# Kernel tuning notes

Measured on AMD Instinct MI355X. Metric: run time of the kernel, lower is better.

## Reference

```python
import jax, jax.numpy as jnp
import numpy as np

D_MODEL = 2048
N_HEADS = 16
HEAD_DIM = D_MODEL // N_HEADS
D_FF = 4 * D_MODEL
BATCH = 2
SEQ = 2048
LN_EPS = 1e-5


def setup_inputs() -> dict:
    key = jax.random.key(0)
    ks = jax.random.split(key, 12)
    s = 0.02
    return {
        "x": jax.random.normal(ks[0], (BATCH, SEQ, D_MODEL), dtype=jnp.float32),
        "alibi_bias": jax.random.normal(ks[1], (N_HEADS, SEQ, SEQ), dtype=jnp.float32),
        "W_q": jax.random.normal(ks[2], (D_MODEL, D_MODEL), dtype=jnp.float32) * s,
        "W_k": jax.random.normal(ks[3], (D_MODEL, D_MODEL), dtype=jnp.float32) * s,
        "W_v": jax.random.normal(ks[4], (D_MODEL, D_MODEL), dtype=jnp.float32) * s,
        "W_o": jax.random.normal(ks[5], (D_MODEL, D_MODEL), dtype=jnp.float32) * s,
        "ln1_g": jnp.ones((D_MODEL,), dtype=jnp.float32),
        "ln1_b": jnp.zeros((D_MODEL,), dtype=jnp.float32),
        "ln2_g": jnp.ones((D_MODEL,), dtype=jnp.float32),
        "ln2_b": jnp.zeros((D_MODEL,), dtype=jnp.float32),
        "ffn_w1": jax.random.normal(ks[6], (D_MODEL, D_FF), dtype=jnp.float32) * s,
        "ffn_b1": jnp.zeros((D_FF,), dtype=jnp.float32),
        "ffn_w2": jax.random.normal(ks[7], (D_FF, D_MODEL), dtype=jnp.float32) * s,
        "ffn_b2": jnp.zeros((D_MODEL,), dtype=jnp.float32),
    }


def _layernorm(x, g, b):
    mu = jnp.mean(x, axis=-1, keepdims=True)
    var = jnp.mean(jnp.square(x - mu), axis=-1, keepdims=True)
    return (x - mu) * jax.lax.rsqrt(var + LN_EPS) * g + b


def _mha(x, alibi_bias, W_q, W_k, W_v, W_o):
    B, S, _ = x.shape
    # nn.Linear applies x @ W.T; here W_* are stored as (in, out) so plain matmul.
    q = (x @ W_q).reshape(B, S, N_HEADS, HEAD_DIM).transpose(0, 2, 1, 3)
    k = (x @ W_k).reshape(B, S, N_HEADS, HEAD_DIM).transpose(0, 2, 1, 3)
    v = (x @ W_v).reshape(B, S, N_HEADS, HEAD_DIM).transpose(0, 2, 1, 3)
    q = q / np.sqrt(HEAD_DIM).astype(np.float32)
    scores = jnp.einsum("bhqd,bhkd->bhqk", q, k)  # [B,H,S,S]
    scores = scores + alibi_bias[None]
    causal = jnp.triu(jnp.ones((S, S), dtype=bool), k=1)
    scores = jnp.where(causal, jnp.finfo(scores.dtype).min, scores)
    attn = jax.nn.softmax(scores, axis=-1)
    out = jnp.einsum("bhqk,bhkd->bhqd", attn, v)
    out = out.transpose(0, 2, 1, 3).reshape(B, S, D_MODEL)
    return out @ W_o


def reference(x, alibi_bias, W_q, W_k, W_v, W_o, ln1_g, ln1_b, ln2_g, ln2_b,
              ffn_w1, ffn_b1, ffn_w2, ffn_b2):
    # Attention block (pre-LN, residual); dropout is identity in eval mode.
    h = x + _mha(_layernorm(x, ln1_g, ln1_b), alibi_bias, W_q, W_k, W_v, W_o)
    # FFN block
    n2 = _layernorm(h, ln2_g, ln2_b)
    ffn = jax.nn.gelu(n2 @ ffn_w1 + ffn_b1, approximate=False) @ ffn_w2 + ffn_b2
    return h + ffn
```

## Files before the change

kernel.cpp:

```cpp
#include <hip/hip_runtime.h>
#include <math.h>

#define DM   2048
#define DFF  8192
#define NH   16
#define HD   128
#define SEQ  2048
#define MROWS 4096

typedef __attribute__((ext_vector_type(4))) float  f32x4;
typedef __attribute__((ext_vector_type(8))) __bf16 bf16x8;
typedef __attribute__((ext_vector_type(4))) short  short4_t;

#define VMCNT(n) asm volatile("s_waitcnt vmcnt(" #n ")" ::: "memory")
#define LGKM0()  asm volatile("s_waitcnt lgkmcnt(0)" ::: "memory")
#define SBAR()   asm volatile("s_barrier" ::: "memory")

__device__ inline unsigned short f2bf(float f) {
  union { float f; unsigned int u; } x; x.f = f;
  unsigned int r = x.u + 0x7FFFu + ((x.u >> 16) & 1u);
  return (unsigned short)(r >> 16);
}

__device__ inline void gload16(const void* g, void* l) {
  __builtin_amdgcn_global_load_lds(
      (const __attribute__((address_space(1))) unsigned int*)g,
      (__attribute__((address_space(3))) unsigned int*)l, 16, 0, 0);
}

__global__ __launch_bounds__(256) void ln_kernel(
    const float* __restrict__ in, const float* __restrict__ gw,
    const float* __restrict__ bw, unsigned short* __restrict__ out)
{
  const int row = blockIdx.x;
  const float* xr = in + (size_t)row * DM;
  const int t = threadIdx.x, lane = t & 63, w = t >> 6;
  float4 v0 = ((const float4*)xr)[t];
  float4 v1 = ((const float4*)xr)[t + 256];
  float s = v0.x+v0.y+v0.z+v0.w + v1.x+v1.y+v1.z+v1.w;
  float s2 = v0.x*v0.x+v0.y*v0.y+v0.z*v0.z+v0.w*v0.w
           + v1.x*v1.x+v1.y*v1.y+v1.z*v1.z+v1.w*v1.w;
  #pragma unroll
  for (int off = 32; off; off >>= 1) { s += __shfl_xor(s, off); s2 += __shfl_xor(s2, off); }
  __shared__ float rs[4], rs2[4];
  if (lane == 0) { rs[w] = s; rs2[w] = s2; }
  __syncthreads();
  s = rs[0] + rs[1] + rs[2] + rs[3];
  s2 = rs2[0] + rs2[1] + rs2[2] + rs2[3];
  const float mu = s * (1.0f / DM);
  const float var = s2 * (1.0f / DM) - mu * mu;
  const float rstd = rsqrtf(var + 1e-5f);
  float4 g0 = ((const float4*)gw)[t],     b0 = ((const float4*)bw)[t];
  float4 g1 = ((const float4*)gw)[t+256], b1 = ((const float4*)bw)[t+256];
  unsigned short* o = out + (size_t)row * DM;
  int i0 = t * 4, i1 = (t + 256) * 4;
  o[i0+0] = f2bf((v0.x-mu)*rstd*g0.x + b0.x);
  o[i0+1] = f2bf((v0.y-mu)*rstd*g0.y + b0.y);
  o[i0+2] = f2bf((v0.z-mu)*rstd*g0.z + b0.z);
  o[i0+3] = f2bf((v0.w-mu)*rstd*g0.w + b0.w);
  o[i1+0] = f2bf((v1.x-mu)*rstd*g1.x + b1.x);
  o[i1+1] = f2bf((v1.y-mu)*rstd*g1.y + b1.y);
  o[i1+2] = f2bf((v1.z-mu)*rstd*g1.z + b1.z);
  o[i1+3] = f2bf((v1.w-mu)*rstd*g1.w + b1.w);
}

__global__ void transpose_kernel(const float* __restrict__ in,
                                 unsigned short* __restrict__ out,
                                 int nrows, int ncols)
{
  __shared__ float tile[32][33];
  const int bx = blockIdx.x * 32;
  const int by = blockIdx.y * 32;
  const int tx = threadIdx.x, ty = threadIdx.y;
  #pragma unroll
  for (int i = ty; i < 32; i += 8)
    tile[i][tx] = in[(size_t)(by + i) * ncols + bx + tx];
  __syncthreads();
  #pragma unroll
  for (int i = ty; i < 32; i += 8)
    out[(size_t)(bx + i) * nrows + by + tx] = f2bf(tile[tx][i]);
}

__global__ void transpose4_kernel(const float* __restrict__ w0,
                                  const float* __restrict__ w1,
                                  const float* __restrict__ w2,
                                  const float* __restrict__ w3,
                                  unsigned short* __restrict__ out)
{
  __shared__ float tile[32][33];
  const float* srcs[4] = {w0, w1, w2, w3};
  const float* in = srcs[blockIdx.z];
  unsigned short* o = out + (size_t)blockIdx.z * DM * DM;
  const int bx = blockIdx.x * 32;
  const int by = blockIdx.y * 32;
  const int tx = threadIdx.x, ty = threadIdx.y;
  #pragma unroll
  for (int i = ty; i < 32; i += 8)
    tile[i][tx] = in[(size_t)(by + i) * DM + bx + tx];
  __syncthreads();
  #pragma unroll
  for (int i = ty; i < 32; i += 8)
    o[(size_t)(bx + i) * DM + by + tx] = f2bf(tile[tx][i]);
}

enum { EPA_QK = 0, EPA_FFN1 = 1 };

#define MFMA16_256(MB_, BV_, NB_)                                                 \
    _Pragma("unroll")                                                             \
    for (int kk = 0; kk < 2; kk++)                                                \
      _Pragma("unroll")                                                           \
      for (int mf = 0; mf < 4; mf++)                                              \
        _Pragma("unroll")                                                         \
        for (int nf = 0; nf < 2; nf++)                                            \
          acc[(MB_) + mf][(NB_) + nf] = __builtin_amdgcn_mfma_f32_16x16x32_bf16(  \
              a[mf][kk], BV_[nf][kk], acc[(MB_) + mf][(NB_) + nf], 0, 0, 0);

#define G256_TILE(T_, S_)                                                         \
  {                                                                               \
    const unsigned short* Ls = lds[S_];                                           \
    _Pragma("unroll")                                                             \
    for (int mf = 0; mf < 4; mf++) {                                              \
      a[mf][0] = *(const bf16x8*)&Ls[abase + mf * 1024 + xo0];                    \
      a[mf][1] = *(const bf16x8*)&Ls[abase + mf * 1024 + xo1];                    \
    }                                                                             \
    _Pragma("unroll")                                                             \
    for (int nf = 0; nf < 2; nf++) {                                              \
      b0[nf][0] = *(const bf16x8*)&Ls[bbase + nf * 1024 + xo0];                   \
      b0[nf][1] = *(const bf16x8*)&Ls[bbase + nf * 1024 + xo1];                   \
    }                                                                             \
    if ((T_) + 1 < NT) stageB((T_) + 1, 1, (S_) ^ 1);                             \
    SBAR();                                                                       \
    __builtin_amdgcn_s_setprio(1);                                                \
    MFMA16_256(0, b0, 0);                                                         \
    __builtin_amdgcn_s_setprio(0);                                                \
    LGKM0();                                                                      \
    SBAR();                                                                       \
    _Pragma("unroll")                                                             \
    for (int nf = 0; nf < 2; nf++) {                                              \
      b1[nf][0] = *(const bf16x8*)&Ls[bbase + 2048 + nf * 1024 + xo0];            \
      b1[nf][1] = *(const bf16x8*)&Ls[bbase + 2048 + nf * 1024 + xo1];            \
    }                                                                             \
    if ((T_) + 2 < NT) stageA((T_) + 2, 0, S_);                                   \
    SBAR();                                                                       \
    __builtin_amdgcn_s_setprio(1);                                                \
    MFMA16_256(0, b1, 2);                                                         \
    __builtin_amdgcn_s_setprio(0);                                                \
    LGKM0();                                                                      \
    SBAR();                                                                       \
    _Pragma("unroll")                                                             \
    for (int mf = 0; mf < 4; mf++) {                                              \
      a[mf][0] = *(const bf16x8*)&Ls[abase + 4096 + mf * 1024 + xo0];             \
      a[mf][1] = *(const bf16x8*)&Ls[abase + 4096 + mf * 1024 + xo1];             \
    }                                                                             \
    if ((T_) + 2 < NT) stageB((T_) + 2, 0, S_);                                   \
    SBAR();                                                                       \
    __builtin_amdgcn_s_setprio(1);                                                \
    MFMA16_256(4, b0, 0);                                                         \
    __builtin_amdgcn_s_setprio(0);                                                \
    LGKM0();                                                                      \
    SBAR();                                                                       \
    if ((T_) + 2 < NT) stageA((T_) + 2, 1, S_);                                   \
    __builtin_amdgcn_s_setprio(1);                                                \
    MFMA16_256(4, b1, 2);                                                         \
    __builtin_amdgcn_s_setprio(0);                                                \
    if ((T_) + 2 < NT) { VMCNT(6); } else { VMCNT(0); }                           \
    SBAR();                                                                       \
  }

template <int MODE>
__global__ __launch_bounds__(512, 2) void gemm256_kernel(
    const unsigned short* __restrict__ A,
    const unsigned short* __restrict__ Bt,
    int K, int N,
    const float* __restrict__ bias,
    void* __restrict__ out)
{
  __shared__ unsigned short lds[2][32768];

  const int t = threadIdx.x;
  const int w = t >> 6, lane = t & 63;
  const int wm = w >> 2, wn = w & 3;
  const int c = lane & 15, g = lane >> 4;

  const long bm = (long)blockIdx.x * 256;
  const long bn = (long)blockIdx.y * 256;
  const int NT = K >> 6;
  const size_t ks = (size_t)K;

  const int tr  = t >> 3;
  const int tc8 = (t & 7) * 8;
  const int sch = ((t & 7) ^ (tr & 7)) * 8;

  auto stageA = [&](int T, int mh, int s) {
    const int r0 = mh * 64 + tr;
    gload16(A + (bm + r0) * ks + T * 64 + sch,       &lds[s][r0 * 64 + tc8]);
    gload16(A + (bm + r0 + 128) * ks + T * 64 + sch, &lds[s][(r0 + 128) * 64 + tc8]);
  };
  auto stageB = [&](int T, int nh, int s) {
    const int r0 = nh * 32 + (tr & 31) + (tr >> 5) * 64;
    gload16(Bt + (bn + r0) * ks + T * 64 + sch,       &lds[s][16384 + r0 * 64 + tc8]);
    gload16(Bt + (bn + r0 + 128) * ks + T * 64 + sch, &lds[s][16384 + (r0 + 128) * 64 + tc8]);
  };

  f32x4 acc[8][4];
  #pragma unroll
  for (int i = 0; i < 8; i++)
    #pragma unroll
    for (int j = 0; j < 4; j++) acc[i][j] = (f32x4){0.f, 0.f, 0.f, 0.f};

  const int xo0 = ((0 + g) ^ (c & 7)) * 8;
  const int xo1 = ((4 + g) ^ (c & 7)) * 8;
  const int abase = (wm * 128 + c) * 64;
  const int bbase = 16384 + (wn * 64 + c) * 64;

  stageA(0, 0, 0); stageB(0, 0, 0); stageA(0, 1, 0); stageB(0, 1, 0);
  stageA(1, 0, 1); stageB(1, 0, 1); stageA(1, 1, 1);
  VMCNT(6);
  SBAR();

  bf16x8 a[4][2], b0[2][2], b1[2][2];

  for (int T = 0; T < NT; T += 2) {
    G256_TILE(T, 0);
    G256_TILE(T + 1, 1);
  }

  #pragma unroll
  for (int mf = 0; mf < 8; mf++) {
    const long row0 = bm + wm * 128 + mf * 16 + g * 4;
    #pragma unroll
    for (int nf = 0; nf < 4; nf++) {
      const long col = bn + wn * 64 + nf * 16 + c;
      #pragma unroll
      for (int r = 0; r < 4; r++) {
        const long row = row0 + r;
        float v = acc[mf][nf][r];
        if constexpr (MODE == EPA_QK) {
          const int slot = (int)(col >> 11);
          const long cc = col & 2047;
          const long hh = cc >> 7, dd = cc & 127;
          const long bb = row >> 11, ss = row & 2047;
          unsigned short* o = (unsigned short*)out;
          if (slot == 0)
            o[((bb * NH + hh) * SEQ + ss) * HD + dd] = f2bf(v * 0.08838834764831845f);
          else
            o[8388608 + ((bb * NH + hh) * SEQ + ss) * HD + dd] = f2bf(v);
        } else {
          float u = v + bias[col];
          float y = 0.7978845608028654f * (u + 0.044715f * u * u * u);
          float e = __expf(-2.0f * fabsf(y));
          float th = (1.0f - e) / (1.0f + e);
          th = (y < 0.0f) ? -th : th;
          ((unsigned short*)out)[row * (long)N + col] = f2bf(0.5f * u * (1.0f + th));
        }
      }
    }
  }
}

enum { EPB_V = 0, EPB_WO = 1, EPB_FFN2 = 2 };

#define MFMA16_128(NH_)                                                           \
    _Pragma("unroll")                                                             \
    for (int kk = 0; kk < 2; kk++)                                                \
      _Pragma("unroll")                                                           \
      for (int mh = 0; mh < 2; mh++)                                              \
        _Pragma("unroll")                                                         \
        for (int m = 0; m < 2; m++)                                               \
          _Pragma("unroll")                                                       \
          for (int n = 0; n < 2; n++)                                             \
            acc[mh][NH_][m][n] = __builtin_amdgcn_mfma_f32_16x16x32_bf16(         \
                a[mh][m][kk], b[n][kk], acc[mh][NH_][m][n], 0, 0, 0);

#define G128_TILE(T_, S_)                                                         \
  {                                                                               \
    const unsigned short* LA  = lds[S_][0];                                       \
    const unsigned short* LB0 = lds[S_][1];                                       \
    const unsigned short* LB1 = lds[S_][2];                                       \
    _Pragma("unroll")                                                             \
    for (int mh = 0; mh < 2; mh++)                                                \
      _Pragma("unroll")                                                           \
      for (int m = 0; m < 2; m++) {                                               \
        a[mh][m][0] = *(const bf16x8*)&LA[arow + mh * 2048 + m * 1024 + k0o];     \
        a[mh][m][1] = *(const bf16x8*)&LA[arow + mh * 2048 + m * 1024 + k1o];     \
      }                                                                           \
    _Pragma("unroll")                                                             \
    for (int n = 0; n < 2; n++) {                                                 \
      b[n][0] = *(const bf16x8*)&LB0[brow + n * 1024 + k0o];                      \
      b[n][1] = *(const bf16x8*)&LB0[brow + n * 1024 + k1o];                      \
    }                                                                             \
    if ((T_) + 1 < NT) stB((T_) + 1, 1, (S_) ^ 1);                                \
    SBAR();                                                                       \
    __builtin_amdgcn_s_setprio(1);                                                \
    MFMA16_128(0);                                                                \
    __builtin_amdgcn_s_setprio(0);                                                \
    LGKM0();                                                                      \
    SBAR();                                                                       \
    _Pragma("unroll")                                                             \
    for (int n = 0; n < 2; n++) {                                                 \
      b[n][0] = *(const bf16x8*)&LB1[brow + n * 1024 + k0o];                      \
      b[n][1] = *(const bf16x8*)&LB1[brow + n * 1024 + k1o];                      \
    }                                                                             \
    if ((T_) + 2 < NT) { stA((T_) + 2, S_); stB((T_) + 2, 0, S_); }               \
    SBAR();                                                                       \
    __builtin_amdgcn_s_setprio(1);                                                \
    MFMA16_128(1);                                                                \
    __builtin_amdgcn_s_setprio(0);                                                \
    LGKM0();                                                                      \
    if ((T_) + 2 < NT) { VMCNT(4); } else { VMCNT(0); }                           \
    SBAR();                                                                       \
  }

template <int MODE>
__global__ __launch_bounds__(512, 2) void gemm128_kernel(
    const unsigned short* __restrict__ A,
    const unsigned short* __restrict__ Bt,
    int K, int N,
    const float* __restrict__ res,
    const float* __restrict__ bias,
    void* __restrict__ out)
{
  __shared__ unsigned short lds[2][3][8192];

  const int t = threadIdx.x;
  const int w = t >> 6, lane = t & 63;
  const int wm = w >> 2, wn = w & 3;
  const int c = lane & 15, g = lane >> 4;
  const int l3 = lane >> 3, l7 = lane & 7;

  const long bm = (long)blockIdx.x * 128;
  const long bn = (long)blockIdx.y * 256;
  const int NT = K >> 6;
  const size_t Ksz = (size_t)K;

  const int scol = (l7 ^ l3) * 8;
  const int r0a = w * 16;

  auto stA = [&](int T, int s) {
    unsigned short* d = &lds[s][0][r0a * 64];
    #pragma unroll
    for (int j = 0; j < 2; j++)
      gload16(A + (bm + r0a + j * 8 + l3) * Ksz + T * 64 + scol, d + j * 512);
  };
  auto stB = [&](int T, int nh, int s) {
    unsigned short* d = &lds[s][1 + nh][r0a * 64];
    #pragma unroll
    for (int j = 0; j < 2; j++)
      gload16(Bt + (bn + nh * 128 + r0a + j * 8 + l3) * Ksz + T * 64 + scol, d + j * 512);
  };

  f32x4 acc[2][2][2][2];
  #pragma unroll
  for (int i = 0; i < 2; i++)
    #pragma unroll
    for (int jq = 0; jq < 2; jq++)
      #pragma unroll
      for (int m = 0; m < 2; m++)
        #pragma unroll
        for (int n = 0; n < 2; n++) acc[i][jq][m][n] = (f32x4){0.f, 0.f, 0.f, 0.f};

  stA(0, 0); stB(0, 0, 0); stB(0, 1, 0);
  stA(1, 1); stB(1, 0, 1);
  VMCNT(4);
  SBAR();

  const int arow = (wm * 64 + c) * 64;
  const int brow = (wn * 32 + c) * 64;
  const int k0o = (g ^ (c & 7)) * 8;
  const int k1o = ((4 | g) ^ (c & 7)) * 8;

  bf16x8 a[2][2][2], b[2][2];

  for (int T = 0; T < NT; T += 2) {
    G128_TILE(T, 0);
    G128_TILE(T + 1, 1);
  }

  #pragma unroll
  for (int mh = 0; mh < 2; mh++)
    #pragma unroll
    for (int nh = 0; nh < 2; nh++)
      #pragma unroll
      for (int m = 0; m < 2; m++)
        #pragma unroll
        for (int n = 0; n < 2; n++) {
          const long row0 = bm + wm * 64 + mh * 32 + m * 16 + g * 4;
          const long col  = bn + nh * 128 + wn * 32 + n * 16 + c;
          #pragma unroll
          for (int r = 0; r < 4; r++) {
            const long row = row0 + r;
            float v = acc[mh][nh][m][n][r];
            if constexpr (MODE == EPB_V) {
              const long hh = col >> 7, dd = col & 127;
              const long bb = row >> 11, ss = row & 2047;
              ((unsigned short*)out)[((bb * NH + hh) * HD + dd) * SEQ + ss] = f2bf(v);
            } else if constexpr (MODE == EPB_WO) {
              ((float*)out)[row * DM + col] = res[row * DM + col] + v;
            } else {
              ((float*)out)[row * DM + col] = res[row * DM + col] + v + bias[col];
            }
          }
        }
}

__global__ __launch_bounds__(256) void attn_kernel(
    const unsigned short* __restrict__ Q,
    const unsigned short* __restrict__ Kg,
    const unsigned short* __restrict__ Vt,
    const float* __restrict__ alibi,
    unsigned short* __restrict__ Out)
{
  __shared__ unsigned short lds[2][16384];

  const int bh = blockIdx.x;
  const int h = bh & (NH - 1);
  const int b = bh >> 4;
  const int j = blockIdx.y;
  const int t = threadIdx.x;
  const int w = t >> 6;
  const int lane = t & 63;
  const int c = lane & 15, g = lane >> 4;
  const int cx = (c & 7) << 4;

  const char* KpB = (const char*)(Kg + (size_t)bh * SEQ * HD);
  const char* VpB = (const char*)(Vt + (size_t)bh * SEQ * HD);
  const unsigned short* Qp = Q + (size_t)bh * SEQ * HD;
  const float* Ah = alibi + (size_t)h * SEQ * SEQ;

  #pragma unroll 1
  for (int half = 0; half < 2; half++) {
    const int cidx = half ? (31 - j) : j;
    const int nt = cidx + 1;
    const int qb = cidx * 64;
    const int q0 = qb + w * 16, qc = q0 + c;

    bf16x8 qf[4];
    #pragma unroll
    for (int dt = 0; dt < 4; dt++)
      qf[dt] = *(const bf16x8*)(Qp + (size_t)qc * HD + dt * 32 + g * 8);

    f32x4 oacc[8];
    #pragma unroll
    for (int d = 0; d < 8; d++) oacc[d] = (f32x4){0.f, 0.f, 0.f, 0.f};
    float m_run = -1e30f, s_run = 0.f;
    const float* Ap = Ah + (size_t)qc * SEQ;

    auto stage = [&](int tt, unsigned short* dst) {
      const size_t kvo = (size_t)tt * 64;
      #pragma unroll
      for (int k = 0; k < 8; k++) {
        const int o = w * 8192 + k * 1024 + lane * 16;
        if (w < 2) {
          const int so = o ^ (((o >> 8) & 7) << 4);
          gload16(KpB + kvo * 256 + so, dst + ((w * 8192 + k * 1024) >> 1));
        } else {
          const int o2 = o - 16384;
          const int d = o2 >> 7, win = o2 & 127;
          gload16(VpB + (size_t)d * 4096 + kvo * 2 + (win ^ ((d & 7) << 4)),
                  dst + ((w * 8192 + k * 1024) >> 1));
        }
      }
    };

    stage(0, lds[0]);
    __syncthreads();
    int buf = 0;

    for (int tt = 0; tt < nt; tt++) {
      if (tt + 1 < nt) stage(tt + 1, lds[buf ^ 1]);
      const unsigned short* LK = lds[buf];
      const unsigned short* LV = lds[buf] + 8192;
      const int kv0 = tt * 64;

      f32x4 sc[4];
      #pragma unroll
      for (int st = 0; st < 4; st++) sc[st] = (f32x4){0.f, 0.f, 0.f, 0.f};
      #pragma unroll
      for (int dt = 0; dt < 4; dt++)
        #pragma unroll
        for (int st = 0; st < 4; st++) {
          bf16x8 kf = *(const bf16x8*)&LK[(st * 4096 + c * 256 + ((dt * 64 + g * 16) ^ cx)) >> 1];
          sc[st] = __builtin_amdgcn_mfma_f32_16x16x32_bf16(kf, qf[dt], sc[st], 0, 0, 0);
        }

      float4 al[4];
      #pragma unroll
      for (int st = 0; st < 4; st++) al[st] = *(const float4*)(Ap + kv0 + st * 16 + g * 4);
      float scr[16];
      #pragma unroll
      for (int st = 0; st < 4; st++) {
        scr[st*4+0] = (kv0 + st*16 + g*4 + 0 > qc) ? -1e30f : sc[st][0] + al[st].x;
        scr[st*4+1] = (kv0 + st*16 + g*4 + 1 > qc) ? -1e30f : sc[st][1] + al[st].y;
        scr[st*4+2] = (kv0 + st*16 + g*4 + 2 > qc) ? -1e30f : sc[st][2] + al[st].z;
        scr[st*4+3] = (kv0 + st*16 + g*4 + 3 > qc) ? -1e30f : sc[st][3] + al[st].w;
      }

      float tm = scr[0];
      #pragma unroll
      for (int i = 1; i < 16; i++) tm = fmaxf(tm, scr[i]);
      tm = fmaxf(tm, __shfl_xor(tm, 16));
      tm = fmaxf(tm, __shfl_xor(tm, 32));
      const float m_new = fmaxf(m_run, tm);
      const float corr = __expf(m_run - m_new);
      float pv[16]; float ps = 0.f;
      #pragma unroll
      for (int i = 0; i < 16; i++) { pv[i] = __expf(scr[i] - m_new); ps += pv[i]; }
      ps += __shfl_xor(ps, 16);
      ps += __shfl_xor(ps, 32);
      s_run = s_run * corr + ps;
      m_run = m_new;

      short4_t pf[4];
      #pragma unroll
      for (int st = 0; st < 4; st++) {
        pf[st][0] = (short)f2bf(pv[st*4+0]); pf[st][1] = (short)f2bf(pv[st*4+1]);
        pf[st][2] = (short)f2bf(pv[st*4+2]); pf[st][3] = (short)f2bf(pv[st*4+3]);
      }

      float cf[4];
      #pragma unroll
      for (int r = 0; r < 4; r++) cf[r] = __shfl(corr, g * 4 + r);

      #pragma unroll
      for (int dt = 0; dt < 8; dt++) {
        f32x4 o = oacc[dt];
        o[0] *= cf[0]; o[1] *= cf[1]; o[2] *= cf[2]; o[3] *= cf[3];
        #pragma unroll
        for (int st = 0; st < 4; st++) {
          short4_t vf = *(const short4_t*)&LV[((dt * 16 + c) * 128 + ((st * 32 + g * 8) ^ cx)) >> 1];
          o = __builtin_amdgcn_mfma_f32_16x16x16bf16_1k(pf[st], vf, o, 0, 0, 0);
        }
        oacc[dt] = o;
      }

      __syncthreads();
      buf ^= 1;
    }

    float inv[4];
    #pragma unroll
    for (int r = 0; r < 4; r++) inv[r] = 1.0f / __shfl(s_run, g * 4 + r);
    #pragma unroll
    for (int dt = 0; dt < 8; dt++)
      #pragma unroll
      for (int r = 0; r < 4; r++)
        Out[(size_t)(b * SEQ + q0 + g * 4 + r) * DM + h * HD + dt * 16 + c] =
            f2bf(oacc[dt][r] * inv[r]);
  }
}

extern "C" void kernel_launch(void* const* d_in, const int* in_sizes, int n_in,
                              void* d_out, int out_size, void* d_ws, size_t ws_size,
                              hipStream_t stream) {
  const float* x     = (const float*)d_in[0];
  const float* alibi = (const float*)d_in[1];
  const float* Wq    = (const float*)d_in[2];
  const float* Wk    = (const float*)d_in[3];
  const float* Wv    = (const float*)d_in[4];
  const float* Wo    = (const float*)d_in[5];
  const float* ln1g  = (const float*)d_in[6];
  const float* ln1b  = (const float*)d_in[7];
  const float* ln2g  = (const float*)d_in[8];
  const float* ln2b  = (const float*)d_in[9];
  const float* w1    = (const float*)d_in[10];
  const float* b1    = (const float*)d_in[11];
  const float* w2    = (const float*)d_in[12];
  const float* b2    = (const float*)d_in[13];

  char* ws = (char*)d_ws;
  float*          hbuf = (float*)(ws);
  unsigned short* xn   = (unsigned short*)(ws + (32ull  << 20));
  unsigned short* qb   = (unsigned short*)(ws + (48ull  << 20));
  unsigned short* kb   = (unsigned short*)(ws + (64ull  << 20));
  unsigned short* vt   = (unsigned short*)(ws + (80ull  << 20));
  unsigned short* ao   = (unsigned short*)(ws + (96ull  << 20));
  unsigned short* wt   = (unsigned short*)(ws + (112ull << 20));
  unsigned short* a1   = (unsigned short*)(ws + (48ull  << 20));

  dim3 blk256(256);
  dim3 blk512(512);
  dim3 tb(32, 8);

  ln_kernel<<<MROWS, blk256, 0, stream>>>(x, ln1g, ln1b, xn);
  transpose4_kernel<<<dim3(DM/32, DM/32, 4), tb, 0, stream>>>(Wq, Wk, Wv, Wo, wt);

  gemm256_kernel<EPA_QK><<<dim3(MROWS/256, (2*DM)/256), blk512, 0, stream>>>(
      xn, wt, DM, 2*DM, nullptr, qb);
  gemm128_kernel<EPB_V><<<dim3(MROWS/128, DM/256), blk512, 0, stream>>>(
      xn, wt + 2ull * DM * DM, DM, DM, nullptr, nullptr, vt);

  attn_kernel<<<dim3(NH * 2, 16), blk256, 0, stream>>>(qb, kb, vt, alibi, ao);

  gemm128_kernel<EPB_WO><<<dim3(MROWS/128, DM/256), blk512, 0, stream>>>(
      ao, wt + 3ull * DM * DM, DM, DM, x, nullptr, hbuf);

  ln_kernel<<<MROWS, blk256, 0, stream>>>(hbuf, ln2g, ln2b, xn);

  transpose_kernel<<<dim3(DFF/32, DM/32), tb, 0, stream>>>(w1, wt, DM, DFF);
  gemm256_kernel<EPA_FFN1><<<dim3(MROWS/256, DFF/256), blk512, 0, stream>>>(
      xn, wt, DM, DFF, b1, a1);

  transpose_kernel<<<dim3(DM/32, DFF/32), tb, 0, stream>>>(w2, wt, DFF, DM);
  gemm128_kernel<EPB_FFN2><<<dim3(MROWS/128, DM/256), blk512, 0, stream>>>(
      a1, wt, DFF, DM, hbuf, b2, (float*)d_out);
}
```

Baseline: 656.1 us.

## Reorder GEMM256 inner loop into k-half phases with restaged prefetch

Restructures the 256x256 bf16 GEMM tile loop so each phase loads one k-half (xo0 or xo1) of A and all four B fragments, instead of both k-halves with half of B. The global-to-LDS staging is reshuffled: the remaining half of tile T+1 is issued early, and both A and B halves of T+2 are issued together in the last phase, with adjusted vmcnt waits. This lowers register pressure for fragments (a[4], b[4]) and changes the load/compute interleaving. B fragments are reused across two phases, and the prefetch distance and LDS read pattern change, which could affect latency hiding.

```diff
diff --git a/kernel.cpp b/kernel.cpp
--- a/kernel.cpp
+++ b/kernel.cpp
@@ -105,65 +105,66 @@
 
 enum { EPA_QK = 0, EPA_FFN1 = 1 };
 
-#define MFMA16_256(MB_, BV_, NB_)                                                 \
-    _Pragma("unroll")                                                             \
-    for (int kk = 0; kk < 2; kk++)                                                \
+#define MFMA16Q(MB_)                                                              \
+    _Pragma("unroll")                                                             \
+    for (int mf = 0; mf < 4; mf++)                                                \
       _Pragma("unroll")                                                           \
-      for (int mf = 0; mf < 4; mf++)                                              \
-        _Pragma("unroll")                                                         \
-        for (int nf = 0; nf < 2; nf++)                                            \
-          acc[(MB_) + mf][(NB_) + nf] = __builtin_amdgcn_mfma_f32_16x16x32_bf16(  \
-              a[mf][kk], BV_[nf][kk], acc[(MB_) + mf][(NB_) + nf], 0, 0, 0);
+      for (int nf = 0; nf < 4; nf++)                                              \
+        acc[(MB_) + mf][nf] = __builtin_amdgcn_mfma_f32_16x16x32_bf16(            \
+            a[mf], b[nf], acc[(MB_) + mf][nf], 0, 0, 0);
 
 #define G256_TILE(T_, S_)                                                         \
   {                                                                               \
     const unsigned short* Ls = lds[S_];                                           \
-    _Pragma("unroll")                                                             \
-    for (int mf = 0; mf < 4; mf++) {                                              \
-      a[mf][0] = *(const bf16x8*)&Ls[abase + mf * 1024 + xo0];                    \
-      a[mf][1] = *(const bf16x8*)&Ls[abase + mf * 1024 + xo1];                    \
-    }                                                                             \
-    _Pragma("unroll")                                                             \
-    for (int nf = 0; nf < 2; nf++) {                                              \
-      b0[nf][0] = *(const bf16x8*)&Ls[bbase + nf * 1024 + xo0];                   \
-      b0[nf][1] = *(const bf16x8*)&Ls[bbase + nf * 1024 + xo1];                   \
-    }                                                                             \
-    if ((T_) + 1 < NT) stageB((T_) + 1, 1, (S_) ^ 1);                             \
+                                                     \
+    _Pragma("unroll")                                                             \
+    for (int mf = 0; mf < 4; mf++)                                                \
+      a[mf] = *(const bf16x8*)&Ls[abase + mf * 1024 + xo0];                       \
+    _Pragma("unroll")                                                             \
+    for (int nf = 0; nf < 4; nf++)                                                \
+      b[nf] = *(const bf16x8*)&Ls[bbase + nf * 1024 + xo0];                       \
+    if ((T_) + 1 < NT) stageA((T_) + 1, 1, (S_) ^ 1);                             \
     SBAR();                                                                       \
     __builtin_amdgcn_s_setprio(1);                                                \
-    MFMA16_256(0, b0, 0);                                                         \
+    MFMA16Q(0);                                                                   \
     __builtin_amdgcn_s_setprio(0);                                                \
     LGKM0();                                                                      \
     SBAR();                                                                       \
-    _Pragma("unroll")                                                             \
-    for (int nf = 0; nf < 2; nf++) {                                              \
-      b1[nf][0] = *(const bf16x8*)&Ls[bbase + 2048 + nf * 1024 + xo0];            \
-      b1[nf][1] = *(const bf16x8*)&Ls[bbase + 2048 + nf * 1024 + xo1];            \
-    }                                                                             \
-    if ((T_) + 2 < NT) stageA((T_) + 2, 0, S_);                                   \
+                                                     \
+    _Pragma("unroll")                                                             \
+    for (int mf = 0; mf < 4; mf++)                                                \
+      a[mf] = *(const bf16x8*)&Ls[abase + 4096 + mf * 1024 + xo0];                \
+    if ((T_) + 1 < NT) stageB((T_) + 1, 1, (S_) ^ 1);                             \
     SBAR();                                                                       \
     __builtin_amdgcn_s_setprio(1);                                                \
-    MFMA16_256(0, b1, 2);                                                         \
+    MFMA16Q(4);                                                                   \
     __builtin_amdgcn_s_setprio(0);                                                \
     LGKM0();                                                                      \
     SBAR();                                                                       \
-    _Pragma("unroll")                                                             \
-    for (int mf = 0; mf < 4; mf++) {                                              \
-      a[mf][0] = *(const bf16x8*)&Ls[abase + 4096 + mf * 1024 + xo0];             \
-      a[mf][1] = *(const bf16x8*)&Ls[abase + 4096 + mf * 1024 + xo1];             \
-    }                                                                             \
-    if ((T_) + 2 < NT) stageB((T_) + 2, 0, S_);                                   \
+                                                     \
+    _Pragma("unroll")                                                             \
+    for (int mf = 0; mf < 4; mf++)                                                \
+      a[mf] = *(const bf16x8*)&Ls[abase + mf * 1024 + xo1];                       \
+    _Pragma("unroll")                                                             \
+    for (int nf = 0; nf < 4; nf++)                                                \
+      b[nf] = *(const bf16x8*)&Ls[bbase + nf * 1024 + xo1];                       \
     SBAR();                                                                       \
     __builtin_amdgcn_s_setprio(1);                                                \
-    MFMA16_256(4, b0, 0);                                                         \
+    MFMA16Q(0);                                                                   \
     __builtin_amdgcn_s_setprio(0);                                                \
     LGKM0();                                                                      \
     SBAR();                                                                       \
-    if ((T_) + 2 < NT) stageA((T_) + 2, 1, S_);                                   \
+                                                     \
+    _Pragma("unroll")                                                             \
+    for (int mf = 0; mf < 4; mf++)                                                \
+      a[mf] = *(const bf16x8*)&Ls[abase + 4096 + mf * 1024 + xo1];                \
+    if ((T_) + 2 < NT) { stageA((T_) + 2, 0, S_); stageB((T_) + 2, 0, S_); }      \
+    SBAR();                                                                       \
     __builtin_amdgcn_s_setprio(1);                                                \
-    MFMA16_256(4, b1, 2);                                                         \
+    MFMA16Q(4);                                                                   \
     __builtin_amdgcn_s_setprio(0);                                                \
-    if ((T_) + 2 < NT) { VMCNT(6); } else { VMCNT(0); }                           \
+    LGKM0();                                                                      \
+    if ((T_) + 2 < NT) { VMCNT(4); } else { VMCNT(0); }                           \
     SBAR();                                                                       \
   }
 
@@ -214,11 +215,11 @@
   const int bbase = 16384 + (wn * 64 + c) * 64;
 
   stageA(0, 0, 0); stageB(0, 0, 0); stageA(0, 1, 0); stageB(0, 1, 0);
-  stageA(1, 0, 1); stageB(1, 0, 1); stageA(1, 1, 1);
-  VMCNT(6);
+  stageA(1, 0, 1); stageB(1, 0, 1);
+  VMCNT(4);
   SBAR();
 
-  bf16x8 a[4][2], b0[2][2], b1[2][2];
+  bf16x8 a[4], b[4];
 
   for (int T = 0; T < NT; T += 2) {
     G256_TILE(T, 0);
```

Result: no change. 653.5 us (-0.4%).
